# Kernel tuning notes

Measured on AMD Instinct MI355X. Metric: run time of the kernel, lower is better.

Reference implementation:

```python
import jax, jax.numpy as jnp
import numpy as np

DIM = 256   # feat channels (init dim)
K = 32      # top-k neighbors (init k)
EPS = 1e-12 # torch F.normalize eps


def setup_inputs() -> dict:
    key = jax.random.key(0)
    # channels = DIM feat + 64 pos-encoding channels
    feat_pos = jax.random.normal(key, (16, 320, 32, 32), dtype=jnp.float32)
    return {"feat_pos": feat_pos}


def reference(feat_pos):
    b, ct, h, w = feat_pos.shape
    n = h * w
    # (b, c_total, h, w) -> (b, n, c_total)
    x = feat_pos.reshape(b, ct, n).transpose(0, 2, 1)
    feat = x[:, :, :DIM]          # (b, n, c)
    pos = x[:, :, DIM:]           # (b, n, p)
    # L2-normalize pos (torch F.normalize semantics: divide by max(norm, eps))
    pos = pos / jnp.maximum(jnp.linalg.norm(pos, axis=-1, keepdims=True), EPS)
    # pairwise cosine similarity (b, n, n)
    sim = jnp.einsum('bnd,bmd->bnm', pos, pos)
    # top-k neighbors per token (sorted descending, same as torch.topk)
    topksim, topkid = jax.lax.top_k(sim, K)          # (b, n, k)
    bidx = jnp.arange(b)[:, None, None]
    topkfeat = feat[bidx, topkid]                    # (b, n, k, c)
    attn = jax.nn.softmax(topksim, axis=-1)          # (b, n, k)
    out = jnp.einsum('bnk,bnkc->bnc', attn, topkfeat)  # (b, n, c)
    return out.reshape(b, h, w, DIM).transpose(0, 3, 1, 2)  # (b, c, h, w)
```

## Files before the change

kernel.cpp:

```cpp
#include <hip/hip_runtime.h>
#include <math.h>

#define CT    320
#define NPTS  1024
#define DFEAT 256
#define DPOS  64
#define KSEL  32

__global__ void gnn_rnj(const float* __restrict__ in, float* __restrict__ rnjg) {
  const int b     = blockIdx.x;
  const int batch = b >> 2;
  const int j     = ((b & 3) << 8) + threadIdx.x;
  const float* __restrict__ pbase = in + (size_t)batch * CT * NPTS + (size_t)DFEAT * NPTS;
  float s = 0.f;
#pragma unroll 8
  for (int d = 0; d < DPOS; ++d) {
    const float x = pbase[(size_t)d * NPTS + j];
    s = fmaf(x, x, s);
  }
  rnjg[batch * NPTS + j] = 1.0f / fmaxf(sqrtf(s), 1e-12f);
}

#define AROWS 16
#define DCH   2
#define QSTEP 6.103515625e-05f
__global__ __launch_bounds__(256, 4) void gnn_sim_topk(const float* __restrict__ in,
                                                       const float* __restrict__ rnjg,
                                                       float2* __restrict__ pairs) {
  __shared__ float pi[DPOS * 20];
  __shared__ float rnjL[NPTS];
  __shared__ float jt[3][DCH * 1024];
  __shared__ float cand[AROWS][68];

  const int p     = blockIdx.x;
  const int batch = ((p & 7) << 1) | ((p >> 3) & 1);
  const int chunk = p >> 4;
  const int i0    = chunk * AROWS;
  const int tid   = threadIdx.x;
  const int w     = tid >> 6;
  const int lane  = tid & 63;

  const float* __restrict__ pbase = in + (size_t)batch * CT * NPTS + (size_t)DFEAT * NPTS;

  {
    const int i = tid & 15;
    const int d0 = tid >> 4;
#pragma unroll
    for (int pass = 0; pass < 4; ++pass) {
      const int d = pass * 16 + d0;
      pi[d * 20 + i] = pbase[(size_t)d * NPTS + i0 + i];
    }
  }
  *(float4*)&rnjL[tid * 4] = *(const float4*)&rnjg[batch * NPTS + tid * 4];

#define JSTAGE(buf, c)                                                           \
  do {                                                                           \
    const int dd_   = (w >> 1);                                                  \
    const int half_ = (w & 1);                                                   \
    const float* src_ = pbase + (size_t)((c) * DCH + dd_) * NPTS + half_ * 512 + lane * 4; \
    float* dst_ = &jt[buf][dd_ * 1024 + half_ * 512];                            \
    __builtin_amdgcn_global_load_lds(                                            \
        (const __attribute__((address_space(1))) void*)(src_),                   \
        (__attribute__((address_space(3))) void*)(dst_), 16, 0, 0);              \
    __builtin_amdgcn_global_load_lds(                                            \
        (const __attribute__((address_space(1))) void*)(src_ + 256),             \
        (__attribute__((address_space(3))) void*)(dst_ + 256), 16, 0, 0);        \
  } while (0)

  JSTAGE(0, 0);
  JSTAGE(1, 1);
  asm volatile("s_waitcnt vmcnt(2)" ::: "memory");
  __syncthreads();

  float acc[4][16];
#pragma unroll
  for (int r = 0; r < 4; ++r)
#pragma unroll
    for (int s = 0; s < 16; ++s) acc[r][s] = 0.f;

  int cur = 0;
  for (int c = 0; c < DPOS / DCH; ++c) {
#pragma unroll
    for (int dd = 0; dd < DCH; ++dd) {
      const int d = c * DCH + dd;
      const float4 pv4 = *(const float4*)&pi[d * 20 + w * 4];
      const float pr_[4] = {pv4.x, pv4.y, pv4.z, pv4.w};
      float4 jv[4];
#pragma unroll
      for (int u = 0; u < 4; ++u)
        jv[u] = *(const float4*)&jt[cur][dd * 1024 + u * 256 + lane * 4];
#pragma unroll
      for (int r = 0; r < 4; ++r) {
#pragma unroll
        for (int u = 0; u < 4; ++u) {
          acc[r][u*4+0] = fmaf(pr_[r], jv[u].x, acc[r][u*4+0]);
          acc[r][u*4+1] = fmaf(pr_[r], jv[u].y, acc[r][u*4+1]);
          acc[r][u*4+2] = fmaf(pr_[r], jv[u].z, acc[r][u*4+2]);
          acc[r][u*4+3] = fmaf(pr_[r], jv[u].w, acc[r][u*4+3]);
        }
      }
    }
    if (c < DPOS / DCH - 2) {
      const int nbuf = (cur + 2 >= 3) ? cur - 1 : cur + 2;
      JSTAGE(nbuf, c + 2);
      asm volatile("s_waitcnt vmcnt(2)" ::: "memory");
    } else {
      asm volatile("s_waitcnt vmcnt(0)" ::: "memory");
    }
    __syncthreads();
    cur = (cur + 1 >= 3) ? 0 : cur + 1;
  }
#undef JSTAGE

  float4 rv[4];
#pragma unroll
  for (int u = 0; u < 4; ++u) rv[u] = *(const float4*)&rnjL[u * 256 + lane * 4];

#pragma unroll
  for (int r = 0; r < 4; ++r) {
    const int rglob = w * 4 + r;
    const float sc = rnjL[i0 + rglob];
    float v[16];
#pragma unroll
    for (int u = 0; u < 4; ++u) {
      v[u*4+0] = acc[r][u*4+0] * rv[u].x * sc;
      v[u*4+1] = acc[r][u*4+1] * rv[u].y * sc;
      v[u*4+2] = acc[r][u*4+2] * rv[u].z * sc;
      v[u*4+3] = acc[r][u*4+3] * rv[u].w * sc;
    }
    int lo = 0;
#pragma unroll
    for (int bit = 16384; bit >= 1; bit >>= 1) {
      const float thrf = (float)(lo + bit) * QSTEP - 1.0f;
      int cnt = 0;
#pragma unroll
      for (int t = 0; t < 16; ++t) cnt += (int)__popcll(__ballot(v[t] >= thrf));
      if (cnt >= KSEL) lo += bit;
    }
    const float thr_h = (float)(lo + 1) * QSTEP - 1.0f;
    const float thr_l = (float)lo * QSTEP - 1.0f;
    int cbase = 0;
    unsigned cmask = 0u;
#pragma unroll
    for (int t = 0; t < 16; ++t) {
      const bool hi = (v[t] >= thr_h);
      const unsigned long long m = __ballot(hi);
      if (hi) {
        const int pos = cbase + (int)__builtin_amdgcn_mbcnt_hi(
            (unsigned)(m >> 32), __builtin_amdgcn_mbcnt_lo((unsigned)m, 0u));
        const int j = (t >> 2) * 256 + lane * 4 + (t & 3);
        *(float2*)&cand[rglob][2 * pos] = make_float2(v[t], __int_as_float(j));
      }
      cbase += (int)__popcll(m);
      if ((v[t] >= thr_l) && !hi) cmask |= (1u << t);
    }
    const int need = KSEL - cbase;
    for (int it = 0; it < need; ++it) {
      float bv = -2.0f; int bj = 0x7fffffff; int bt = 16;
#pragma unroll
      for (int t = 0; t < 16; ++t) {
        if (((cmask >> t) & 1u) && v[t] > bv) {
          bv = v[t]; bj = (t >> 2) * 256 + lane * 4 + (t & 3); bt = t;
        }
      }
      float rvv = bv; int rj = bj;
#pragma unroll
      for (int s = 1; s < 64; s <<= 1) {
        const float ov = __shfl_xor(rvv, s);
        const int   oj = __shfl_xor(rj, s);
        if (ov > rvv || (ov == rvv && oj < rj)) { rvv = ov; rj = oj; }
      }
      if (bv == rvv && bj == rj) {
        *(float2*)&cand[rglob][2 * (cbase + it)] = make_float2(bv, __int_as_float(bj));
        cmask &= ~(1u << bt);
      }
    }
    {
      const float x = cand[rglob][2 * (lane & 31)];
      float mx = x;
#pragma unroll
      for (int s = 16; s >= 1; s >>= 1) mx = fmaxf(mx, __shfl_xor(mx, s));
      const float e = expf(x - mx);
      float sum = e;
#pragma unroll
      for (int s = 16; s >= 1; s >>= 1) sum += __shfl_xor(sum, s);
      if (lane < KSEL) cand[rglob][2 * lane] = e / sum;
    }
  }
  __syncthreads();

  {
    const int pidx = tid * 2;
    const int r = pidx >> 5, k = pidx & 31;
    const float4 o4 = *(const float4*)&cand[r][2 * k];
    *(float4*)&pairs[((size_t)batch * NPTS + i0 + r) * KSEL + k] = o4;
  }
}

__global__ __launch_bounds__(256, 2) void gnn_gather(const float* __restrict__ in,
                                                     const float2* __restrict__ pairs,
                                                     float* __restrict__ out) {
  __shared__ float fst[4][2][2048];

  const int p     = blockIdx.x;
  const int batch = ((p & 7) << 1) | ((p >> 3) & 1);
  const int chunk = p >> 4;
  const int i0    = chunk * 32;
  const int tid   = threadIdx.x;
  const int w     = tid >> 6;
  const int lane  = tid & 63;
  const int row   = lane & 31;
  const int half  = lane >> 5;

  const float* __restrict__ fbase = in + (size_t)batch * CT * NPTS;

  float a[KSEL]; int jj[KSEL];
  {
    const float4* pr4 = (const float4*)(pairs + ((size_t)batch * NPTS + i0 + row) * KSEL);
#pragma unroll
    for (int q = 0; q < 16; ++q) {
      const float4 o4 = pr4[q];
      a[2*q]   = o4.x; jj[2*q]   = __float_as_int(o4.y) + half * 1024;
      a[2*q+1] = o4.z; jj[2*q+1] = __float_as_int(o4.w) + half * 1024;
    }
  }

#define BSTAGE(buf, ccv)                                                         \
  do {                                                                           \
    _Pragma("unroll")                                                            \
    for (int rr = 0; rr < 2; ++rr) {                                             \
      const int ch = (ccv) * 8 + w * 2 + rr;                                     \
      const float* src = fbase + (size_t)ch * NPTS + lane * 4;                   \
      float* dst = &fst[w][buf][rr * 1024];                                      \
      _Pragma("unroll")                                                          \
      for (int qq = 0; qq < 4; ++qq)                                             \
        __builtin_amdgcn_global_load_lds(                                        \
            (const __attribute__((address_space(1))) void*)(src + qq * 256),     \
            (__attribute__((address_space(3))) void*)(dst + qq * 256), 16, 0, 0);\
    }                                                                            \
  } while (0)

  BSTAGE(0, 0);
  int cur = 0;
  for (int cc = 0; cc < 32; ++cc) {
    if (cc < 31) {
      BSTAGE(cur ^ 1, cc + 1);
      asm volatile("s_waitcnt vmcnt(8)" ::: "memory");
    } else {
      asm volatile("s_waitcnt vmcnt(0)" ::: "memory");
    }
    const float* fb = &fst[w][cur][0];
    float o = 0.f;
#pragma unroll
    for (int k = 0; k < KSEL; ++k)
      o = fmaf(a[k], fb[jj[k]], o);
    const int ch = cc * 8 + w * 2 + half;
    out[((size_t)batch * DFEAT + ch) * NPTS + i0 + row] = o;
    cur ^= 1;
  }
#undef BSTAGE
}

extern "C" void kernel_launch(void* const* d_in, const int* in_sizes, int n_in,
                              void* d_out, int out_size, void* d_ws, size_t ws_size,
                              hipStream_t stream) {
  const float* in = (const float*)d_in[0];
  float* out = (float*)d_out;
  float2* pairs = (float2*)d_ws;
  float*  rnjg  = (float*)((char*)d_ws + (16u << 20) / 4);
  gnn_rnj<<<dim3(64), dim3(256), 0, stream>>>(in, rnjg);
  gnn_sim_topk<<<dim3(1024), dim3(256), 0, stream>>>(in, rnjg, pairs);
  gnn_gather<<<dim3(512), dim3(256), 0, stream>>>(in, pairs, out);
}
```

Measured before the change: 102.3 us.

## Restage gather features as channel-interleaved float4 tiles in LDS per wave

The gather kernel no longer streams two channels per stage into LDS with async global_load_lds. Each wave now loads four channels into registers, transposes them into an interleaved LDS layout, and reads one float4 per neighbor to cover four channels at once. The 32 neighbors are split across the two half-waves and combined with a cross-lane shuffle. This cuts the number of LDS gather reads per output and the loop count, but drops the double-buffered async copy, adds register pressure from the tile array, and needs a swizzled index mapping that has to be correct.

```diff
diff --git a/kernel.cpp b/kernel.cpp
--- a/kernel.cpp
+++ b/kernel.cpp
@@ -200,7 +200,7 @@
 __global__ __launch_bounds__(256, 2) void gnn_gather(const float* __restrict__ in,
                                                      const float2* __restrict__ pairs,
                                                      float* __restrict__ out) {
-  __shared__ float fst[4][2][2048];
+  __shared__ float fst[4][4096];
 
   const int p     = blockIdx.x;
   const int batch = ((p & 7) << 1) | ((p >> 3) & 1);
@@ -210,55 +210,90 @@
   const int w     = tid >> 6;
   const int lane  = tid & 63;
   const int row   = lane & 31;
-  const int half  = lane >> 5;
+  const int khalf = lane >> 5;
+  const int ch0   = w * 64;
 
   const float* __restrict__ fbase = in + (size_t)batch * CT * NPTS;
-
-  float a[KSEL]; int jj[KSEL];
+  float* const fw = &fst[w][0];
+
+  float a16[16]; int jjb[16];
   {
-    const float4* pr4 = (const float4*)(pairs + ((size_t)batch * NPTS + i0 + row) * KSEL);
-#pragma unroll
-    for (int q = 0; q < 16; ++q) {
-      const float4 o4 = pr4[q];
-      a[2*q]   = o4.x; jj[2*q]   = __float_as_int(o4.y) + half * 1024;
-      a[2*q+1] = o4.z; jj[2*q+1] = __float_as_int(o4.w) + half * 1024;
-    }
-  }
-
-#define BSTAGE(buf, ccv)                                                         \
+    const float4* pr4 = (const float4*)(pairs + ((size_t)batch * NPTS + i0 + row) * KSEL)
+                        + khalf * 8;
+#pragma unroll
+    for (int qq = 0; qq < 8; ++qq) {
+      const float4 o = pr4[qq];
+      const int id0 = __float_as_int(o.y);
+      const int id1 = __float_as_int(o.w);
+      a16[2*qq]   = o.x;
+      jjb[2*qq]   = ((((id0 & 3) << 6) | ((id0 >> 2) & 63) | (id0 & ~255)) << 4);
+      a16[2*qq+1] = o.z;
+      jjb[2*qq+1] = ((((id1 & 3) << 6) | ((id1 >> 2) & 63) | (id1 & ~255)) << 4);
+    }
+  }
+
+  float4 tile[4][4];
+
+#define LOADT(pp)                                                                \
   do {                                                                           \
     _Pragma("unroll")                                                            \
-    for (int rr = 0; rr < 2; ++rr) {                                             \
-      const int ch = (ccv) * 8 + w * 2 + rr;                                     \
-      const float* src = fbase + (size_t)ch * NPTS + lane * 4;                   \
-      float* dst = &fst[w][buf][rr * 1024];                                      \
+    for (int it = 0; it < 4; ++it) {                                             \
       _Pragma("unroll")                                                          \
-      for (int qq = 0; qq < 4; ++qq)                                             \
-        __builtin_amdgcn_global_load_lds(                                        \
-            (const __attribute__((address_space(1))) void*)(src + qq * 256),     \
-            (__attribute__((address_space(3))) void*)(dst + qq * 256), 16, 0, 0);\
+      for (int c = 0; c < 4; ++c)                                                \
+        tile[it][c] = *(const float4*)(fbase +                                   \
+            (size_t)(ch0 + (pp) * 4 + c) * NPTS + it * 256 + lane * 4);          \
     }                                                                            \
   } while (0)
 
-  BSTAGE(0, 0);
-  int cur = 0;
-  for (int cc = 0; cc < 32; ++cc) {
-    if (cc < 31) {
-      BSTAGE(cur ^ 1, cc + 1);
-      asm volatile("s_waitcnt vmcnt(8)" ::: "memory");
+#define WRITET()                                                                 \
+  do {                                                                           \
+    _Pragma("unroll")                                                            \
+    for (int it = 0; it < 4; ++it) {                                             \
+      *(float4*)&fw[(256*it + lane) * 4] =                                       \
+          make_float4(tile[it][0].x, tile[it][1].x, tile[it][2].x, tile[it][3].x);\
+      *(float4*)&fw[(256*it + 64 + lane) * 4] =                                  \
+          make_float4(tile[it][0].y, tile[it][1].y, tile[it][2].y, tile[it][3].y);\
+      *(float4*)&fw[(256*it + 128 + lane) * 4] =                                 \
+          make_float4(tile[it][0].z, tile[it][1].z, tile[it][2].z, tile[it][3].z);\
+      *(float4*)&fw[(256*it + 192 + lane) * 4] =                                 \
+          make_float4(tile[it][0].w, tile[it][1].w, tile[it][2].w, tile[it][3].w);\
+    }                                                                            \
+  } while (0)
+
+  LOADT(0);
+  WRITET();
+
+  for (int pp = 0; pp < 16; ++pp) {
+    if (pp < 15) LOADT(pp + 1);
+
+    float4 o4 = make_float4(0.f, 0.f, 0.f, 0.f);
+#pragma unroll
+    for (int kk = 0; kk < 16; ++kk) {
+      const float4 f4 = *(const float4*)((const char*)fw + jjb[kk]);
+      const float ak = a16[kk];
+      o4.x = fmaf(ak, f4.x, o4.x);
+      o4.y = fmaf(ak, f4.y, o4.y);
+      o4.z = fmaf(ak, f4.z, o4.z);
+      o4.w = fmaf(ak, f4.w, o4.w);
+    }
+    o4.x += __shfl_xor(o4.x, 32);
+    o4.y += __shfl_xor(o4.y, 32);
+    o4.z += __shfl_xor(o4.z, 32);
+    o4.w += __shfl_xor(o4.w, 32);
+
+    float* ob = out + ((size_t)batch * DFEAT + ch0 + pp * 4) * NPTS + i0 + row;
+    if (khalf == 0) {
+      ob[0]            = o4.x;
+      ob[(size_t)NPTS] = o4.y;
     } else {
-      asm volatile("s_waitcnt vmcnt(0)" ::: "memory");
-    }
-    const float* fb = &fst[w][cur][0];
-    float o = 0.f;
-#pragma unroll
-    for (int k = 0; k < KSEL; ++k)
-      o = fmaf(a[k], fb[jj[k]], o);
-    const int ch = cc * 8 + w * 2 + half;
-    out[((size_t)batch * DFEAT + ch) * NPTS + i0 + row] = o;
-    cur ^= 1;
-  }
-#undef BSTAGE
+      ob[(size_t)2 * NPTS] = o4.z;
+      ob[(size_t)3 * NPTS] = o4.w;
+    }
+
+    if (pp < 15) WRITET();
+  }
+#undef LOADT
+#undef WRITET
 }
 
 extern "C" void kernel_launch(void* const* d_in, const int* in_sizes, int n_in,
```

Result: faster. 98.92 us, median of 2 (-3.3%).
